# Kernel tuning notes

Measured on AMD Instinct MI355X. Metric: run time of the kernel, lower is better.

The kernel has to match this reference:

```python
import jax, jax.numpy as jnp
import numpy as np
import math

D_MODEL = 2048
N_HEADS = 16
D_HEAD = D_MODEL // N_HEADS
SCALE = 1.0 / math.sqrt(D_HEAD)


def setup_inputs() -> dict:
    key = jax.random.key(0)
    kx, kq, kk, kv, ko = jax.random.split(key, 5)
    x = jax.random.normal(kx, (2, 2048, D_MODEL), dtype=jnp.float32)
    W_q = jax.random.normal(kq, (D_MODEL, D_MODEL), dtype=jnp.float32)
    W_k = jax.random.normal(kk, (D_MODEL, D_MODEL), dtype=jnp.float32)
    W_v = jax.random.normal(kv, (D_MODEL, D_MODEL), dtype=jnp.float32) * math.sqrt(2.0 / D_MODEL)
    W_o = jax.random.normal(ko, (D_MODEL, D_MODEL), dtype=jnp.float32) * math.sqrt(2.0 / D_MODEL)
    return {"x": x, "W_q": W_q, "W_k": W_k, "W_v": W_v, "W_o": W_o}


def reference(x, W_q, W_k, W_v, W_o) -> jnp.ndarray:
    B, S, D = x.shape
    q = (x @ W_q).reshape(B, S, N_HEADS, D_HEAD)  # [b, q, h, dh]
    k = (x @ W_k).reshape(B, S, N_HEADS, D_HEAD)  # [b, k, h, dh]
    v = x @ W_v                                    # [b, k, d_model] (NOT split into heads)
    scores = jnp.einsum('bqhd,bkhd->bhqk', q, k)   # [b, h, q, k]
    # Faithful quirk: additive -1e9 causal mask applied BEFORE the scale.
    mask = jnp.triu(jnp.full((S, S), -1e9, dtype=scores.dtype), k=1)
    scores = (scores + mask) * SCALE
    probs = jax.nn.softmax(scores, axis=-1)
    # Faithful quirk: sums over heads h AND keys k against full-width v.
    out = jnp.einsum('bhqk,bkd->bqd', probs, v)    # [b, q, d_model]
    return out @ W_o
```

## Files before the change

### kernel.cpp

```cpp
#include <hip/hip_runtime.h>

typedef unsigned short u16;
typedef __attribute__((ext_vector_type(8))) short bf16x8;
typedef __attribute__((ext_vector_type(4))) float f32x4;

#define DEV __device__ __forceinline__
#define EXP2(x) __builtin_amdgcn_exp2f(x)
#define LOG2(x) __builtin_amdgcn_logf(x)

DEV u16 f2bf(float f) {
  union { float f; unsigned u; } v; v.f = f;
  unsigned r = v.u + 0x7fffu + ((v.u >> 16) & 1u);
  return (u16)(r >> 16);
}
DEV float bf2f(u16 h) {
  union { unsigned u; float f; } v; v.u = ((unsigned)h) << 16;
  return v.f;
}
DEV f32x4 mfma16(bf16x8 a, bf16x8 b, f32x4 c) {
  return __builtin_amdgcn_mfma_f32_16x16x32_bf16(a, b, c, 0, 0, 0);
}
DEV void cp16(const u16* g, u16* l) {
  __builtin_amdgcn_global_load_lds((__attribute__((address_space(1))) void*)g,
                                   (__attribute__((address_space(3))) void*)l, 16, 0, 0);
}

__global__ __launch_bounds__(256) void split_pair(const float4* __restrict__ x,
                                                  u16* __restrict__ hi, u16* __restrict__ lo) {
  const size_t i = (size_t)blockIdx.x * 256 + threadIdx.x;
  const float4 v = x[i];
  ushort4 h, l;
  h.x = f2bf(v.x); l.x = f2bf(v.x - bf2f(h.x));
  h.y = f2bf(v.y); l.y = f2bf(v.y - bf2f(h.y));
  h.z = f2bf(v.z); l.z = f2bf(v.z - bf2f(h.z));
  h.w = f2bf(v.w); l.w = f2bf(v.w - bf2f(h.w));
  *(ushort4*)&hi[i * 4] = h;
  *(ushort4*)&lo[i * 4] = l;
}

template<bool LO>
__global__ __launch_bounds__(256) void transpose_split(const float* __restrict__ W,
                                                       u16* __restrict__ Th, u16* __restrict__ Tl) {
  __shared__ float t[64][65];
  const int r0 = blockIdx.y * 64, c0 = blockIdx.x * 64;
  const int rr = threadIdx.x >> 4, c4 = (threadIdx.x & 15) * 4;
#pragma unroll
  for (int p = 0; p < 4; ++p) {
    const float4 v = *(const float4*)&W[(size_t)(r0 + p * 16 + rr) * 2048 + c0 + c4];
    t[p * 16 + rr][c4 + 0] = v.x; t[p * 16 + rr][c4 + 1] = v.y;
    t[p * 16 + rr][c4 + 2] = v.z; t[p * 16 + rr][c4 + 3] = v.w;
  }
  __syncthreads();
#pragma unroll
  for (int p = 0; p < 4; ++p) {
    const int cc = p * 16 + rr;
    const float v0 = t[c4 + 0][cc], v1 = t[c4 + 1][cc], v2 = t[c4 + 2][cc], v3 = t[c4 + 3][cc];
    ushort4 h;
    h.x = f2bf(v0); h.y = f2bf(v1); h.z = f2bf(v2); h.w = f2bf(v3);
    *(ushort4*)&Th[(size_t)(c0 + cc) * 2048 + r0 + c4] = h;
    if constexpr (LO) {
      ushort4 l;
      l.x = f2bf(v0 - bf2f(h.x)); l.y = f2bf(v1 - bf2f(h.y));
      l.z = f2bf(v2 - bf2f(h.z)); l.w = f2bf(v3 - bf2f(h.w));
      *(ushort4*)&Tl[(size_t)(c0 + cc) * 2048 + r0 + c4] = l;
    }
  }
}

template<bool SPLIT3, int OUTMODE, bool KLIM>
__global__ __launch_bounds__(256, 2) void gemm_bt(
    const u16* __restrict__ Aph, const u16* __restrict__ Apl,
    const u16* __restrict__ Bph, const u16* __restrict__ Bpl,
    void* __restrict__ C0, void* __restrict__ C1,
    const int M, const int N, const int K, const int bShift) {
  extern __shared__ u16 lds[];
  constexpr int T_AL = 4096;
  constexpr int T_BH = SPLIT3 ? 8192 : 4096;
  constexpr int T_BL = 12288;
  const int tid = threadIdx.x;
  const int wave = tid >> 6, lane = tid & 63;
  const int li = lane & 15, l4 = lane >> 4;
  const int m0 = blockIdx.y * 128, n0 = blockIdx.x * 128;
  const int wr = (wave >> 1) * 64, wc = (wave & 1) * 64;
  const u16* Bh = Bph; const u16* Bl = Bpl;
  if (bShift) { const size_t s = (size_t)(m0 >> 11) * (size_t)bShift; Bh += s; if (SPLIT3) Bl += s; }

  const f32x4 fz = {0.f, 0.f, 0.f, 0.f};
  f32x4 acc[4][4];
#pragma unroll
  for (int m = 0; m < 4; ++m)
#pragma unroll
    for (int n = 0; n < 4; ++n) acc[m][n] = fz;

  const size_t aoff = (size_t)(m0 + (tid >> 2)) * K + (tid & 3) * 8;
  const size_t boff = (size_t)(n0 + (tid >> 2)) * K + (tid & 3) * 8;
  const size_t rstep = (size_t)64 * K;
  const int s0 = tid * 8, s1 = 2048 + tid * 8;
  const int abase = (wr + li) * 32 + l4 * 8;
  const int bbase = (wc + li) * 32 + l4 * 8;
  const int kEnd = KLIM ? ((m0 & 2047) + 128 < K ? (m0 & 2047) + 128 : K) : K;

#pragma unroll 1
  for (int k0 = 0; k0 < kEnd; k0 += 32) {
    cp16(Aph + aoff + k0,         &lds[s0]);
    cp16(Aph + aoff + rstep + k0, &lds[s1]);
    cp16(Bh + boff + k0,          &lds[T_BH + s0]);
    cp16(Bh + boff + rstep + k0,  &lds[T_BH + s1]);
    if constexpr (SPLIT3) {
      cp16(Apl + aoff + k0,         &lds[T_AL + s0]);
      cp16(Apl + aoff + rstep + k0, &lds[T_AL + s1]);
      cp16(Bl + boff + k0,          &lds[T_BL + s0]);
      cp16(Bl + boff + rstep + k0,  &lds[T_BL + s1]);
    }
    __syncthreads();
    bf16x8 af[4], bf_[4];
#pragma unroll
    for (int m = 0; m < 4; ++m) af[m] = *(const bf16x8*)&lds[abase + m * 512];
#pragma unroll
    for (int n = 0; n < 4; ++n) bf_[n] = *(const bf16x8*)&lds[T_BH + bbase + n * 512];
    if constexpr (SPLIT3) {
      bf16x8 alf[4], blf[4];
#pragma unroll
      for (int m = 0; m < 4; ++m) alf[m] = *(const bf16x8*)&lds[T_AL + abase + m * 512];
#pragma unroll
      for (int n = 0; n < 4; ++n) blf[n] = *(const bf16x8*)&lds[T_BL + bbase + n * 512];
#pragma unroll
      for (int m = 0; m < 4; ++m)
#pragma unroll
        for (int n = 0; n < 4; ++n) {
          acc[m][n] = mfma16(af[m], bf_[n], acc[m][n]);
          acc[m][n] = mfma16(af[m], blf[n], acc[m][n]);
          acc[m][n] = mfma16(alf[m], bf_[n], acc[m][n]);
        }
    } else {
#pragma unroll
      for (int m = 0; m < 4; ++m)
#pragma unroll
        for (int n = 0; n < 4; ++n)
          acc[m][n] = mfma16(af[m], bf_[n], acc[m][n]);
    }
    __syncthreads();
  }

#pragma unroll
  for (int m = 0; m < 4; ++m) {
#pragma unroll
    for (int n = 0; n < 4; ++n) {
      const int rg0 = m0 + wr + m * 16 + l4 * 4;
      const int cg  = n0 + wc + n * 16 + li;
      if constexpr (OUTMODE == 0) {
        u16* Ch = (u16*)C0; u16* Cl = (u16*)C1;
#pragma unroll
        for (int r = 0; r < 4; ++r) {
          const float v = acc[m][n][r];
          const u16 h = f2bf(v);
          Ch[(size_t)(rg0 + r) * N + cg] = h;
          Cl[(size_t)(rg0 + r) * N + cg] = f2bf(v - bf2f(h));
        }
      } else if constexpr (OUTMODE == 1) {
        u16* Cs = (u16*)C0;
#pragma unroll
        for (int r = 0; r < 4; ++r) Cs[(size_t)(rg0 + r) * N + cg] = f2bf(acc[m][n][r]);
      } else if constexpr (OUTMODE == 2) {
        u16* Vt = (u16*)C0;
        ushort4 pk;
        pk.x = f2bf(acc[m][n][0]); pk.y = f2bf(acc[m][n][1]);
        pk.z = f2bf(acc[m][n][2]); pk.w = f2bf(acc[m][n][3]);
        *(ushort4*)&Vt[(size_t)(rg0 >> 11) * 4194304 + (size_t)cg * 2048 + (rg0 & 2047)] = pk;
      } else {
        float* Cf = (float*)C0;
#pragma unroll
        for (int r = 0; r < 4; ++r) Cf[(size_t)(rg0 + r) * N + cg] = acc[m][n][r];
      }
    }
  }
}

#define C2EXP 0.1275174381027786f

__global__ __launch_bounds__(256) void attn_lse_part(
    const u16* __restrict__ Qh, const u16* __restrict__ Ql,
    const u16* __restrict__ Kh, const u16* __restrict__ Kl,
    float* __restrict__ Mp, float* __restrict__ Lp) {
  const int j = blockIdx.x, qt = 15 - (int)blockIdx.y, hb = blockIdx.z;
  const int b = hb >> 4, h = hb & 15;
  const int tid = threadIdx.x;
  const int nch = (qt >> 2) + 1;
  if (j >= nch) {
    if (tid < 128) {
      const size_t o = ((size_t)hb * 4 + j) * 2048 + qt * 128 + tid;
      Mp[o] = -3.0e38f; Lp[o] = 0.f;
    }
    return;
  }
  __shared__ __align__(16) u16 kb[16384];
  const int wave = tid >> 6, lane = tid & 63;
  const int li = lane & 15, l4 = lane >> 4;
  const int q0w = qt * 128 + wave * 32;
  const int rs = ((li << 6) | (l4 << 4)) ^ (((li >> 1) & 7) << 4);

  bf16x8 qfh[2][4], qfl[2][4];
#pragma unroll
  for (int mf = 0; mf < 2; ++mf) {
    const size_t qo = ((size_t)(b * 2048 + q0w + mf * 16 + li)) * 2048 + h * 128 + l4 * 8;
#pragma unroll
    for (int ks = 0; ks < 4; ++ks) {
      qfh[mf][ks] = *(const bf16x8*)&Qh[qo + ks * 32];
      qfl[mf][ks] = *(const bf16x8*)&Ql[qo + ks * 32];
    }
  }
  float m[2][4], l[2][4];
#pragma unroll
  for (int mf = 0; mf < 2; ++mf)
#pragma unroll
    for (int r = 0; r < 4; ++r) { m[mf][r] = -3.0e38f; l[mf][r] = 0.f; }

  const int kst = j * 8;
  const int ken = min(j * 8 + 8, qt * 2 + 2);
  const size_t kgbase = ((size_t)b * 2048) * 2048 + h * 128;
  const f32x4 fz = {0.f, 0.f, 0.f, 0.f};

#pragma unroll 1
  for (int t = kst; t < ken; ++t) {
    __syncthreads();
#pragma unroll
    for (int i = 0; i < 4; ++i) {
      const int o = (tid + i * 256) * 16;
      const int op = o ^ (((o >> 7) & 7) << 4);
      const int dck = op >> 12, s = (op >> 6) & 63, dl = (op >> 1) & 31;
      const size_t g = kgbase + (size_t)(t * 64 + s) * 2048 + dck * 32 + dl;
      cp16(Kh + g, kb + (o >> 1));
      cp16(Kl + g, kb + 8192 + (o >> 1));
    }
    __syncthreads();
#pragma unroll
    for (int sn = 0; sn < 4; ++sn) {
      f32x4 a0 = fz, a1 = fz;
#pragma unroll
      for (int ks = 0; ks < 4; ++ks) {
        const bf16x8 kh = *(const bf16x8*)((const char*)kb + ks * 4096 + (sn << 10) + rs);
        const bf16x8 kl = *(const bf16x8*)((const char*)kb + 16384 + ks * 4096 + (sn << 10) + rs);
        a0 = mfma16(qfh[0][ks], kh, a0);
        a0 = mfma16(qfh[0][ks], kl, a0);
        a0 = mfma16(qfl[0][ks], kh, a0);
        a1 = mfma16(qfh[1][ks], kh, a1);
        a1 = mfma16(qfh[1][ks], kl, a1);
        a1 = mfma16(qfl[1][ks], kh, a1);
      }
      const int kg = t * 64 + sn * 16 + li;
#pragma unroll
      for (int r = 0; r < 4; ++r) {
        if (kg <= q0w + l4 * 4 + r) {
          const float mn = fmaxf(m[0][r], a0[r]);
          l[0][r] = l[0][r] * EXP2((m[0][r] - mn) * C2EXP) + EXP2((a0[r] - mn) * C2EXP);
          m[0][r] = mn;
        }
        if (kg <= q0w + 16 + l4 * 4 + r) {
          const float mn = fmaxf(m[1][r], a1[r]);
          l[1][r] = l[1][r] * EXP2((m[1][r] - mn) * C2EXP) + EXP2((a1[r] - mn) * C2EXP);
          m[1][r] = mn;
        }
      }
    }
  }
#pragma unroll
  for (int off = 1; off <= 8; off <<= 1) {
#pragma unroll
    for (int mf = 0; mf < 2; ++mf)
#pragma unroll
      for (int r = 0; r < 4; ++r) {
        const float om = __shfl_xor(m[mf][r], off, 64);
        const float ol = __shfl_xor(l[mf][r], off, 64);
        const float mn = fmaxf(m[mf][r], om);
        l[mf][r] = l[mf][r] * EXP2((m[mf][r] - mn) * C2EXP) + ol * EXP2((om - mn) * C2EXP);
        m[mf][r] = mn;
      }
  }
  if (li == 0) {
#pragma unroll
    for (int mf = 0; mf < 2; ++mf)
#pragma unroll
      for (int r = 0; r < 4; ++r) {
        const size_t o = ((size_t)hb * 4 + j) * 2048 + q0w + mf * 16 + l4 * 4 + r;
        Mp[o] = m[mf][r];
        Lp[o] = l[mf][r];
      }
  }
}

__global__ __launch_bounds__(256) void attn_lse_merge(
    const float* __restrict__ Mp, const float* __restrict__ Lp, float* __restrict__ LSE) {
  const int id = blockIdx.x * 256 + threadIdx.x;
  const int q = id & 2047, hb = id >> 11;
  const size_t base = (size_t)hb * 4 * 2048 + q;
  float m = Mp[base], l = Lp[base];
#pragma unroll
  for (int jj = 1; jj < 4; ++jj) {
    const float om = Mp[base + jj * 2048];
    const float ol = Lp[base + jj * 2048];
    const float mn = fmaxf(m, om);
    l = l * EXP2((m - mn) * C2EXP) + ol * EXP2((om - mn) * C2EXP);
    m = mn;
  }
  LSE[(size_t)hb * 2048 + q] = m * C2EXP + LOG2(l);
}

__global__ __launch_bounds__(256) void attn_psum(
    const u16* __restrict__ Qh, const u16* __restrict__ Ql,
    const u16* __restrict__ Kh, const u16* __restrict__ Kl,
    const float* __restrict__ LSE, u16* __restrict__ Psum) {
  const int kt = blockIdx.x, qt = blockIdx.y, b = blockIdx.z;
  const int q0 = qt * 128, k0 = kt * 128;
  const int tid = threadIdx.x;

  if (kt > qt) {
    const size_t o = ((size_t)(b * 2048 + q0 + (tid >> 1))) * 2048 + k0 + (tid & 1) * 64;
    const uint4 z = {0u, 0u, 0u, 0u};
#pragma unroll
    for (int j = 0; j < 8; ++j) *(uint4*)&Psum[o + j * 8] = z;
    return;
  }

  extern __shared__ u16 kb2[];
  const int wave = tid >> 6, lane = tid & 63;
  const int li = lane & 15, l4 = lane >> 4;
  const int q0w = q0 + wave * 32;
  const int rs = ((li << 6) | (l4 << 4)) ^ (((li >> 1) & 7) << 4);
  const int snmax = (kt == qt) ? (wave * 2 + 2) : 8;

  const f32x4 fz = {0.f, 0.f, 0.f, 0.f};
  f32x4 ps[2][8];
#pragma unroll
  for (int mf = 0; mf < 2; ++mf)
#pragma unroll
    for (int sn = 0; sn < 8; ++sn) ps[mf][sn] = fz;

  const size_t kgbase = ((size_t)(b * 2048 + k0)) * 2048;
  const size_t qbase0 = ((size_t)(b * 2048 + q0w + li)) * 2048 + l4 * 8;
  const size_t qbase1 = qbase0 + (size_t)16 * 2048;
  const size_t lbase  = (size_t)(b * 16) * 2048 + q0w + l4 * 4;

#pragma unroll 1
  for (int h = 0; h < 16; ++h) {
    __syncthreads();
#pragma unroll
    for (int i = 0; i < 8; ++i) {
      const int o = (tid + i * 256) * 16;
      const int op = o ^ (((o >> 7) & 7) << 4);
      const int dck = op >> 13, s = (op >> 6) & 127, dl = (op >> 1) & 31;
      const size_t g = kgbase + (size_t)s * 2048 + h * 128 + dck * 32 + dl;
      cp16(Kh + g, kb2 + (o >> 1));
      cp16(Kl + g, kb2 + 16384 + (o >> 1));
    }
    bf16x8 qfh0[4], qfl0[4], qfh1[4], qfl1[4];
    float clse[2][4];
#pragma unroll
    for (int ks = 0; ks < 4; ++ks) {
      qfh0[ks] = *(const bf16x8*)&Qh[qbase0 + (size_t)h * 128 + ks * 32];
      qfl0[ks] = *(const bf16x8*)&Ql[qbase0 + (size_t)h * 128 + ks * 32];
      qfh1[ks] = *(const bf16x8*)&Qh[qbase1 + (size_t)h * 128 + ks * 32];
      qfl1[ks] = *(const bf16x8*)&Ql[qbase1 + (size_t)h * 128 + ks * 32];
    }
#pragma unroll
    for (int mf = 0; mf < 2; ++mf)
#pragma unroll
      for (int r = 0; r < 4; ++r)
        clse[mf][r] = LSE[lbase + (size_t)h * 2048 + mf * 16 + r];
    __syncthreads();

#pragma unroll
    for (int sn = 0; sn < 8; ++sn) {
      if (sn < snmax) {
        f32x4 a0 = fz, a1 = fz;
#pragma unroll
        for (int ks = 0; ks < 4; ++ks) {
          const bf16x8 kh = *(const bf16x8*)((const char*)kb2 + ks * 8192 + (sn << 10) + rs);
          const bf16x8 kl = *(const bf16x8*)((const char*)kb2 + 32768 + ks * 8192 + (sn << 10) + rs);
          a0 = mfma16(qfh0[ks], kh, a0);
          a0 = mfma16(qfh0[ks], kl, a0);
          a0 = mfma16(qfl0[ks], kh, a0);
          a1 = mfma16(qfh1[ks], kh, a1);
          a1 = mfma16(qfh1[ks], kl, a1);
          a1 = mfma16(qfl1[ks], kh, a1);
        }
        const int kg = k0 + sn * 16 + li;
#pragma unroll
        for (int r = 0; r < 4; ++r) {
          if (kg <= q0w + l4 * 4 + r)      ps[0][sn][r] += EXP2(a0[r] * C2EXP - clse[0][r]);
          if (kg <= q0w + 16 + l4 * 4 + r) ps[1][sn][r] += EXP2(a1[r] * C2EXP - clse[1][r]);
        }
      }
    }
  }

#pragma unroll
  for (int mf = 0; mf < 2; ++mf)
#pragma unroll
    for (int sn = 0; sn < 8; ++sn) {
      const size_t o0 = ((size_t)(b * 2048 + q0w + mf * 16 + l4 * 4)) * 2048 + k0 + sn * 16 + li;
#pragma unroll
      for (int r = 0; r < 4; ++r) Psum[o0 + (size_t)r * 2048] = f2bf(ps[mf][sn][r]);
    }
}

extern "C" void kernel_launch(void* const* d_in, const int* in_sizes, int n_in,
                              void* d_out, int out_size, void* d_ws, size_t ws_size,
                              hipStream_t stream) {
  (void)in_sizes; (void)n_in; (void)out_size; (void)ws_size;
  const float* x  = (const float*)d_in[0];
  const float* Wq = (const float*)d_in[1];
  const float* Wk = (const float*)d_in[2];
  const float* Wv = (const float*)d_in[3];
  const float* Wo = (const float*)d_in[4];
  u16* ws = (u16*)d_ws;
  const size_t E8 = 8388608, E4 = 4194304;
  u16* xh = ws;
  u16* xl = ws + E8;
  u16* Qh = ws + 2 * E8;
  u16* Ql = ws + 3 * E8;
  u16* Kh = ws + 4 * E8;
  u16* Kl = ws + 5 * E8;
  u16* Vt = ws + 6 * E8;
  u16* WTh = ws + 7 * E8;
  u16* WTl = ws + 7 * E8 + E4;
  u16* WTb = ws + 7 * E8 + 2 * E4;
  float* LSEf = (float*)WTl;
  float* Mp   = LSEf + 65536;
  float* Lp   = Mp + 262144;
  u16* Psum = xl;
  u16* out1 = xh;

  split_pair<<<8192, 256, 0, stream>>>((const float4*)x, xh, xl);

  dim3 tg(32, 32);
  dim3 gg(16, 32);

  transpose_split<true ><<<tg, 256, 0, stream>>>(Wq, WTh, WTl);
  gemm_bt<true, 0, false><<<gg, 256, 32768, stream>>>(xh, xl, WTh, WTl, Qh, Ql, 4096, 2048, 2048, 0);

  transpose_split<true ><<<tg, 256, 0, stream>>>(Wk, WTh, WTl);
  gemm_bt<true, 0, false><<<gg, 256, 32768, stream>>>(xh, xl, WTh, WTl, Kh, Kl, 4096, 2048, 2048, 0);

  transpose_split<false><<<tg, 256, 0, stream>>>(Wv, WTb, nullptr);
  gemm_bt<false, 2, false><<<gg, 256, 16384, stream>>>(xh, nullptr, WTb, nullptr, Vt, nullptr, 4096, 2048, 2048, 0);

  attn_lse_part<<<dim3(4, 16, 32), 256, 0, stream>>>(Qh, Ql, Kh, Kl, Mp, Lp);
  attn_lse_merge<<<256, 256, 0, stream>>>(Mp, Lp, LSEf);
  attn_psum<<<dim3(16, 16, 2), 256, 65536, stream>>>(Qh, Ql, Kh, Kl, LSEf, Psum);

  gemm_bt<false, 1, true><<<gg, 256, 16384, stream>>>(Psum, nullptr, Vt, nullptr, out1, nullptr, 4096, 2048, 2048, 4194304);

  transpose_split<false><<<tg, 256, 0, stream>>>(Wo, WTb, nullptr);
  gemm_bt<false, 3, false><<<gg, 256, 16384, stream>>>(out1, nullptr, WTb, nullptr, d_out, nullptr, 4096, 2048, 2048, 0);
}
```

Baseline: 602.1 us.

## Batch Q/K projections in one launch and refine attention work partitioning

Result: slower. 704.1 us (+16.9%).

```diff
diff --git a/kernel.cpp b/kernel.cpp
--- a/kernel.cpp
+++ b/kernel.cpp
@@ -71,12 +71,15 @@
 __global__ __launch_bounds__(256, 2) void gemm_bt(
     const u16* __restrict__ Aph, const u16* __restrict__ Apl,
     const u16* __restrict__ Bph, const u16* __restrict__ Bpl,
+    const u16* __restrict__ Bph2, const u16* __restrict__ Bpl2,
     void* __restrict__ C0, void* __restrict__ C1,
+    void* __restrict__ C0b, void* __restrict__ C1b,
     const int M, const int N, const int K, const int bShift) {
   extern __shared__ u16 lds[];
   constexpr int T_AL = 4096;
   constexpr int T_BH = SPLIT3 ? 8192 : 4096;
   constexpr int T_BL = 12288;
+  if (blockIdx.z) { Bph = Bph2; Bpl = Bpl2; C0 = C0b; C1 = C1b; }
   const int tid = threadIdx.x;
   const int wave = tid >> 6, lane = tid & 63;
   const int li = lane & 15, l4 = lane >> 4;
@@ -185,10 +188,10 @@
   const int j = blockIdx.x, qt = 15 - (int)blockIdx.y, hb = blockIdx.z;
   const int b = hb >> 4, h = hb & 15;
   const int tid = threadIdx.x;
-  const int nch = (qt >> 2) + 1;
+  const int nch = (2 * qt + 5) >> 2;
   if (j >= nch) {
     if (tid < 128) {
-      const size_t o = ((size_t)hb * 4 + j) * 2048 + qt * 128 + tid;
+      const size_t o = ((size_t)hb * 8 + j) * 2048 + qt * 128 + tid;
       Mp[o] = -3.0e38f; Lp[o] = 0.f;
     }
     return;
@@ -215,8 +218,8 @@
 #pragma unroll
     for (int r = 0; r < 4; ++r) { m[mf][r] = -3.0e38f; l[mf][r] = 0.f; }
 
-  const int kst = j * 8;
-  const int ken = min(j * 8 + 8, qt * 2 + 2);
+  const int kst = 4 * j;
+  const int ken = min(4 * j + 4, 2 * qt + 2);
   const size_t kgbase = ((size_t)b * 2048) * 2048 + h * 128;
   const f32x4 fz = {0.f, 0.f, 0.f, 0.f};
 
@@ -233,34 +236,51 @@
       cp16(Kl + g, kb + 8192 + (o >> 1));
     }
     __syncthreads();
+
+    f32x4 av0[4], av1[4];
 #pragma unroll
     for (int sn = 0; sn < 4; ++sn) {
-      f32x4 a0 = fz, a1 = fz;
-#pragma unroll
-      for (int ks = 0; ks < 4; ++ks) {
-        const bf16x8 kh = *(const bf16x8*)((const char*)kb + ks * 4096 + (sn << 10) + rs);
-        const bf16x8 kl = *(const bf16x8*)((const char*)kb + 16384 + ks * 4096 + (sn << 10) + rs);
-        a0 = mfma16(qfh[0][ks], kh, a0);
-        a0 = mfma16(qfh[0][ks], kl, a0);
-        a0 = mfma16(qfl[0][ks], kh, a0);
-        a1 = mfma16(qfh[1][ks], kh, a1);
-        a1 = mfma16(qfh[1][ks], kl, a1);
-        a1 = mfma16(qfl[1][ks], kh, a1);
-      }
-      const int kg = t * 64 + sn * 16 + li;
-#pragma unroll
-      for (int r = 0; r < 4; ++r) {
-        if (kg <= q0w + l4 * 4 + r) {
-          const float mn = fmaxf(m[0][r], a0[r]);
-          l[0][r] = l[0][r] * EXP2((m[0][r] - mn) * C2EXP) + EXP2((a0[r] - mn) * C2EXP);
-          m[0][r] = mn;
-        }
-        if (kg <= q0w + 16 + l4 * 4 + r) {
-          const float mn = fmaxf(m[1][r], a1[r]);
-          l[1][r] = l[1][r] * EXP2((m[1][r] - mn) * C2EXP) + EXP2((a1[r] - mn) * C2EXP);
-          m[1][r] = mn;
-        }
-      }
+      if (64 * t + 16 * sn <= q0w + 31) {
+        f32x4 a0 = fz, a1 = fz;
+#pragma unroll
+        for (int ks = 0; ks < 4; ++ks) {
+          const bf16x8 kh = *(const bf16x8*)((const char*)kb + ks * 4096 + (sn << 10) + rs);
+          const bf16x8 kl = *(const bf16x8*)((const char*)kb + 16384 + ks * 4096 + (sn << 10) + rs);
+          a0 = mfma16(qfh[0][ks], kh, a0);
+          a0 = mfma16(qfh[0][ks], kl, a0);
+          a0 = mfma16(qfl[0][ks], kh, a0);
+          a1 = mfma16(qfh[1][ks], kh, a1);
+          a1 = mfma16(qfh[1][ks], kl, a1);
+          a1 = mfma16(qfl[1][ks], kh, a1);
+        }
+        av0[sn] = a0; av1[sn] = a1;
+      }
+    }
+#pragma unroll
+    for (int r = 0; r < 4; ++r) {
+      float mx0 = m[0][r], mx1 = m[1][r];
+      float am0[4], am1[4];
+#pragma unroll
+      for (int sn = 0; sn < 4; ++sn) {
+        if (64 * t + 16 * sn <= q0w + 31) {
+          const int kg = t * 64 + sn * 16 + li;
+          am0[sn] = (kg <= q0w + l4 * 4 + r)      ? av0[sn][r] : -3.0e38f;
+          am1[sn] = (kg <= q0w + 16 + l4 * 4 + r) ? av1[sn][r] : -3.0e38f;
+          mx0 = fmaxf(mx0, am0[sn]);
+          mx1 = fmaxf(mx1, am1[sn]);
+        }
+      }
+      float s0 = 0.f, s1 = 0.f;
+#pragma unroll
+      for (int sn = 0; sn < 4; ++sn) {
+        if (64 * t + 16 * sn <= q0w + 31) {
+          s0 += EXP2((am0[sn] - mx0) * C2EXP);
+          s1 += EXP2((am1[sn] - mx1) * C2EXP);
+        }
+      }
+      l[0][r] = l[0][r] * EXP2((m[0][r] - mx0) * C2EXP) + s0;
+      l[1][r] = l[1][r] * EXP2((m[1][r] - mx1) * C2EXP) + s1;
+      m[0][r] = mx0; m[1][r] = mx1;
     }
   }
 #pragma unroll
@@ -281,7 +301,7 @@
     for (int mf = 0; mf < 2; ++mf)
 #pragma unroll
       for (int r = 0; r < 4; ++r) {
-        const size_t o = ((size_t)hb * 4 + j) * 2048 + q0w + mf * 16 + l4 * 4 + r;
+        const size_t o = ((size_t)hb * 8 + j) * 2048 + q0w + mf * 16 + l4 * 4 + r;
         Mp[o] = m[mf][r];
         Lp[o] = l[mf][r];
       }
@@ -292,10 +312,10 @@
     const float* __restrict__ Mp, const float* __restrict__ Lp, float* __restrict__ LSE) {
   const int id = blockIdx.x * 256 + threadIdx.x;
   const int q = id & 2047, hb = id >> 11;
-  const size_t base = (size_t)hb * 4 * 2048 + q;
+  const size_t base = (size_t)hb * 8 * 2048 + q;
   float m = Mp[base], l = Lp[base];
 #pragma unroll
-  for (int jj = 1; jj < 4; ++jj) {
+  for (int jj = 1; jj < 8; ++jj) {
     const float om = Mp[base + jj * 2048];
     const float ol = Lp[base + jj * 2048];
     const float mn = fmaxf(m, om);
@@ -310,30 +330,31 @@
     const u16* __restrict__ Kh, const u16* __restrict__ Kl,
     const float* __restrict__ LSE, u16* __restrict__ Psum) {
   const int kt = blockIdx.x, qt = blockIdx.y, b = blockIdx.z;
-  const int q0 = qt * 128, k0 = kt * 128;
+  const int q0 = qt * 128, k0 = kt * 64;
   const int tid = threadIdx.x;
 
-  if (kt > qt) {
-    const size_t o = ((size_t)(b * 2048 + q0 + (tid >> 1))) * 2048 + k0 + (tid & 1) * 64;
+  if (k0 > q0 + 127) {
+    const size_t o = ((size_t)(b * 2048 + q0 + (tid >> 1))) * 2048 + k0 + (tid & 1) * 32;
     const uint4 z = {0u, 0u, 0u, 0u};
 #pragma unroll
-    for (int j = 0; j < 8; ++j) *(uint4*)&Psum[o + j * 8] = z;
+    for (int j2 = 0; j2 < 4; ++j2) *(uint4*)&Psum[o + j2 * 8] = z;
     return;
   }
 
-  extern __shared__ u16 kb2[];
+  __shared__ __align__(16) u16 kb[16384];
   const int wave = tid >> 6, lane = tid & 63;
   const int li = lane & 15, l4 = lane >> 4;
   const int q0w = q0 + wave * 32;
   const int rs = ((li << 6) | (l4 << 4)) ^ (((li >> 1) & 7) << 4);
-  const int snmax = (kt == qt) ? (wave * 2 + 2) : 8;
+  int snmax = ((q0w + 31 - k0) >> 4) + 1;
+  snmax = snmax < 0 ? 0 : (snmax > 4 ? 4 : snmax);
 
   const f32x4 fz = {0.f, 0.f, 0.f, 0.f};
-  f32x4 ps[2][8];
+  f32x4 ps[2][4];
 #pragma unroll
   for (int mf = 0; mf < 2; ++mf)
 #pragma unroll
-    for (int sn = 0; sn < 8; ++sn) ps[mf][sn] = fz;
+    for (int sn = 0; sn < 4; ++sn) ps[mf][sn] = fz;
 
   const size_t kgbase = ((size_t)(b * 2048 + k0)) * 2048;
   const size_t qbase0 = ((size_t)(b * 2048 + q0w + li)) * 2048 + l4 * 8;
@@ -344,13 +365,13 @@
   for (int h = 0; h < 16; ++h) {
     __syncthreads();
 #pragma unroll
-    for (int i = 0; i < 8; ++i) {
+    for (int i = 0; i < 4; ++i) {
       const int o = (tid + i * 256) * 16;
       const int op = o ^ (((o >> 7) & 7) << 4);
-      const int dck = op >> 13, s = (op >> 6) & 127, dl = (op >> 1) & 31;
+      const int dck = op >> 12, s = (op >> 6) & 63, dl = (op >> 1) & 31;
       const size_t g = kgbase + (size_t)s * 2048 + h * 128 + dck * 32 + dl;
-      cp16(Kh + g, kb2 + (o >> 1));
-      cp16(Kl + g, kb2 + 16384 + (o >> 1));
+      cp16(Kh + g, kb + (o >> 1));
+      cp16(Kl + g, kb + 8192 + (o >> 1));
     }
     bf16x8 qfh0[4], qfl0[4], qfh1[4], qfl1[4];
     float clse[2][4];
@@ -369,13 +390,13 @@
     __syncthreads();
 
 #pragma unroll
-    for (int sn = 0; sn < 8; ++sn) {
+    for (int sn = 0; sn < 4; ++sn) {
       if (sn < snmax) {
         f32x4 a0 = fz, a1 = fz;
 #pragma unroll
         for (int ks = 0; ks < 4; ++ks) {
-          const bf16x8 kh = *(const bf16x8*)((const char*)kb2 + ks * 8192 + (sn << 10) + rs);
-          const bf16x8 kl = *(const bf16x8*)((const char*)kb2 + 32768 + ks * 8192 + (sn << 10) + rs);
+          const bf16x8 kh = *(const bf16x8*)((const char*)kb + ks * 4096 + (sn << 10) + rs);
+          const bf16x8 kl = *(const bf16x8*)((const char*)kb + 16384 + ks * 4096 + (sn << 10) + rs);
           a0 = mfma16(qfh0[ks], kh, a0);
           a0 = mfma16(qfh0[ks], kl, a0);
           a0 = mfma16(qfl0[ks], kh, a0);
@@ -396,7 +417,7 @@
 #pragma unroll
   for (int mf = 0; mf < 2; ++mf)
 #pragma unroll
-    for (int sn = 0; sn < 8; ++sn) {
+    for (int sn = 0; sn < 4; ++sn) {
       const size_t o0 = ((size_t)(b * 2048 + q0w + mf * 16 + l4 * 4)) * 2048 + k0 + sn * 16 + li;
 #pragma unroll
       for (int r = 0; r < 4; ++r) Psum[o0 + (size_t)r * 2048] = f2bf(ps[mf][sn][r]);
@@ -424,32 +445,39 @@
   u16* WTh = ws + 7 * E8;
   u16* WTl = ws + 7 * E8 + E4;
   u16* WTb = ws + 7 * E8 + 2 * E4;
+  u16* WkTh = Vt;
+  u16* WkTl = Vt + E4;
   float* LSEf = (float*)WTl;
   float* Mp   = LSEf + 65536;
-  float* Lp   = Mp + 262144;
+  float* Lp   = Mp + 524288;
   u16* Psum = xl;
   u16* out1 = xh;
 
   split_pair<<<8192, 256, 0, stream>>>((const float4*)x, xh, xl);
 
   dim3 tg(32, 32);
-  dim3 gg(16, 32);
 
   transpose_split<true ><<<tg, 256, 0, stream>>>(Wq, WTh, WTl);
-  gemm_bt<true, 0, false><<<gg, 256, 32768, stream>>>(xh, xl, WTh, WTl, Qh, Ql, 4096, 2048, 2048, 0);
-
-  transpose_split<true ><<<tg, 256, 0, stream>>>(Wk, WTh, WTl);
-  gemm_bt<true, 0, false><<<gg, 256, 32768, stream>>>(xh, xl, WTh, WTl, Kh, Kl, 4096, 2048, 2048, 0);
-
+  transpose_split<true ><<<tg, 256, 0, stream>>>(Wk, WkTh, WkTl);
   transpose_split<false><<<tg, 256, 0, stream>>>(Wv, WTb, nullptr);
-  gemm_bt<false, 2, false><<<gg, 256, 16384, stream>>>(xh, nullptr, WTb, nullptr, Vt, nullptr, 4096, 2048, 2048, 0);
-
-  attn_lse_part<<<dim3(4, 16, 32), 256, 0, stream>>>(Qh, Ql, Kh, Kl, Mp, Lp);
+
+  gemm_bt<true, 0, false><<<dim3(16, 32, 2), 256, 32768, stream>>>(
+      xh, xl, WTh, WTl, WkTh, WkTl, Qh, Ql, Kh, Kl, 4096, 2048, 2048, 0);
+
+  gemm_bt<false, 2, false><<<dim3(16, 32), 256, 16384, stream>>>(
+      xh, nullptr, WTb, nullptr, nullptr, nullptr, Vt, nullptr, nullptr, nullptr,
+      4096, 2048, 2048, 0);
+
+  attn_lse_part<<<dim3(8, 16, 32), 256, 0, stream>>>(Qh, Ql, Kh, Kl, Mp, Lp);
   attn_lse_merge<<<256, 256, 0, stream>>>(Mp, Lp, LSEf);
-  attn_psum<<<dim3(16, 16, 2), 256, 65536, stream>>>(Qh, Ql, Kh, Kl, LSEf, Psum);
-
-  gemm_bt<false, 1, true><<<gg, 256, 16384, stream>>>(Psum, nullptr, Vt, nullptr, out1, nullptr, 4096, 2048, 2048, 4194304);
+  attn_psum<<<dim3(32, 16, 2), 256, 0, stream>>>(Qh, Ql, Kh, Kl, LSEf, Psum);
+
+  gemm_bt<false, 1, true><<<dim3(16, 32), 256, 16384, stream>>>(
+      Psum, nullptr, Vt, nullptr, nullptr, nullptr, out1, nullptr, nullptr, nullptr,
+      4096, 2048, 2048, 4194304);
 
   transpose_split<false><<<tg, 256, 0, stream>>>(Wo, WTb, nullptr);
-  gemm_bt<false, 3, false><<<gg, 256, 16384, stream>>>(out1, nullptr, WTb, nullptr, d_out, nullptr, 4096, 2048, 2048, 0);
-}
+  gemm_bt<false, 3, false><<<dim3(16, 32), 256, 16384, stream>>>(
+      out1, nullptr, WTb, nullptr, nullptr, nullptr, d_out, nullptr, nullptr, nullptr,
+      4096, 2048, 2048, 0);
+}
```
